# Optimization experiments

Hardware: AMD Instinct MI355X
Metric: run time of the kernel (lower is better)

## Reference

```python
import jax, jax.numpy as jnp
import numpy as np

T, B, E = 1024, 4, 1024
H = 16
D = E // H          # head_dim = 64
L = 16              # max_relative_length


def setup_inputs() -> dict:
    key = jax.random.key(0)
    ks = jax.random.split(key, 4)
    query = jax.random.normal(ks[0], (T, B, E), dtype=jnp.float32)
    # xavier-ish scaled params
    in_proj_weight = jax.random.normal(ks[1], (3 * E, E), dtype=jnp.float32) * (1.0 / np.sqrt(E))
    in_proj_bias = jnp.zeros((3 * E,), dtype=jnp.float32)
    rel_pos_keys = jax.random.normal(ks[2], (2 * L + 1, E), dtype=jnp.float32) * (1.0 / np.sqrt(E))
    out_w = jax.random.normal(ks[3], (E, E), dtype=jnp.float32) * (1.0 / np.sqrt(E))
    out_b = jnp.zeros((E,), dtype=jnp.float32)
    return {"query": query, "in_proj_weight": in_proj_weight, "in_proj_bias": in_proj_bias,
            "rel_pos_keys": rel_pos_keys, "out_w": out_w, "out_b": out_b}


def reference(query, in_proj_weight, in_proj_bias, rel_pos_keys, out_w, out_b):
    t, b, e = query.shape
    scaling = D ** (-0.5)
    # fused qkv projection: [T,B,3E]
    qkv = jnp.einsum('tbe,fe->tbf', query, in_proj_weight) + in_proj_bias
    q, k, v = jnp.split(qkv, 3, axis=-1)
    q = q * scaling
    # [T,B,E] -> [B*H, T, D]
    def heads(x):
        return x.reshape(t, b * H, D).transpose(1, 0, 2)
    q, k, v = heads(q), heads(k), heads(v)
    # clipped relative position matrix [T,T] in [0, 2L]
    r = jnp.arange(t)
    dist = jnp.clip(r[None, :] - r[:, None], -L, L) + L
    # gather relation keys, keep first head_dim channels: [T,T,D]
    rel_k = rel_pos_keys[dist][:, :, :D]
    # scores = q k^T + q . rel_k  (Shaw et al.), [B*H, T, T]
    scores = jnp.einsum('btd,bsd->bts', q, k) + jnp.einsum('btd,tsd->bts', q, rel_k)
    probs = jax.nn.softmax(scores, axis=-1)
    attn = jnp.einsum('bts,bsd->btd', probs, v)      # [B*H, T, D]
    attn = attn.transpose(1, 0, 2).reshape(t, b, e)   # [T, B, E]
    return jnp.einsum('tbe,oe->tbo', attn, out_w) + out_b
```

## Files before the change

kernel.cpp:

```cpp
#include <hip/hip_runtime.h>

typedef __attribute__((ext_vector_type(8))) short short8;
typedef __attribute__((ext_vector_type(4))) float floatx4;


__device__ __forceinline__ short f2bf(float x) {
  union { float f; unsigned u; } cv; cv.f = x;
  unsigned u = cv.u + (0x7FFFu + ((cv.u >> 16) & 1u));
  return (short)(u >> 16);
}

__device__ __forceinline__ floatx4 mfma16(short8 a, short8 b, floatx4 c) {
  return __builtin_amdgcn_mfma_f32_16x16x32_bf16(a, b, c, 0, 0, 0);
}

__device__ __forceinline__ void async_copy16(const void* g, void* l) {
  __builtin_amdgcn_global_load_lds((const __attribute__((address_space(1))) void*)g,
                                   (__attribute__((address_space(3))) void*)l, 16, 0, 0);
}

__global__ void __launch_bounds__(256) convert_all_kernel(
    const float* __restrict__ s0, const float* __restrict__ s1,
    const float* __restrict__ s2,
    short* __restrict__ d0, short* __restrict__ d1, short* __restrict__ d2)
{
  int i = blockIdx.x * 256 + threadIdx.x;
  const float* src; short* dst; int off;
  if (i < 524288)       { src = s0; dst = d0; off = i; }
  else if (i < 917504)  { src = s1; dst = d1; off = i - 524288; }
  else                  { src = s2; dst = d2; off = i - 917504; }
  const float4* s = (const float4*)src;
  float4 a = s[off * 2], b = s[off * 2 + 1];
  short8 o;
  o[0] = f2bf(a.x); o[1] = f2bf(a.y); o[2] = f2bf(a.z); o[3] = f2bf(a.w);
  o[4] = f2bf(b.x); o[5] = f2bf(b.y); o[6] = f2bf(b.z); o[7] = f2bf(b.w);
  *(short8*)(dst + (size_t)off * 8) = o;
}

__device__ __forceinline__ void gemm_stage(
    const short* __restrict__ A, const short* __restrict__ W,
    short* Atile, short* Btile, int m0, int n0, int K, int kk, int tid, int w)
{
  #pragma unroll
  for (int i = 0; i < 2; i++) {
    int seg = i * 256 + tid;
    int row = seg >> 2, p = seg & 3;
    int ck = (p - ((row >> 1) & 3)) & 3;
    async_copy16(A + (size_t)(m0 + row) * K + kk + ck * 8,
                 Atile + (size_t)(i * 256 + w * 64) * 8);
    async_copy16(W + (size_t)(n0 + row) * K + kk + ck * 8,
                 Btile + (size_t)(i * 256 + w * 64) * 8);
  }
}

__device__ __forceinline__ void gemm_core_db(
    const short* __restrict__ A, const short* __restrict__ W,
    short* At, short* Bt,
    int m0, int n0, int K, int tid, floatx4 acc[4][4])
{
  const int lane = tid & 63, w = tid >> 6;
  const int quad = lane >> 4, l16 = lane & 15;
  const int wm = (w >> 1) * 64, wn = (w & 1) * 64;
  #pragma unroll
  for (int mt = 0; mt < 4; mt++)
    #pragma unroll
    for (int nt = 0; nt < 4; nt++) acc[mt][nt] = (floatx4)(0.0f);

  gemm_stage(A, W, At, Bt, m0, n0, K, 0, tid, w);

  for (int kk = 0; kk < K; kk += 32) {
    const int cur = (kk >> 5) & 1;
    short* Ac = At + cur * (128 * 32);
    short* Bc = Bt + cur * (128 * 32);
    __syncthreads();
    if (kk + 32 < K)
      gemm_stage(A, W, At + (1 - cur) * (128 * 32), Bt + (1 - cur) * (128 * 32),
                 m0, n0, K, kk + 32, tid, w);
    short8 af[4], bfr[4];
    #pragma unroll
    for (int mt = 0; mt < 4; mt++) {
      int R = wm + mt * 16 + l16;
      af[mt] = *(const short8*)(Ac + R * 32 + ((quad + (R >> 1)) & 3) * 8);
    }
    #pragma unroll
    for (int nt = 0; nt < 4; nt++) {
      int R = wn + nt * 16 + l16;
      bfr[nt] = *(const short8*)(Bc + R * 32 + ((quad + (R >> 1)) & 3) * 8);
    }
    #pragma unroll
    for (int mt = 0; mt < 4; mt++)
      #pragma unroll
      for (int nt = 0; nt < 4; nt++)
        acc[mt][nt] = mfma16(af[mt], bfr[nt], acc[mt][nt]);
  }
}

__global__ void __launch_bounds__(256) gemm_qkv(
    const short* __restrict__ A, const short* __restrict__ W,
    const float* __restrict__ bias,
    short* __restrict__ q_ws, short* __restrict__ k_ws, short* __restrict__ v_ws)
{
  __shared__ __align__(16) short Atile[2 * 128 * 32];
  __shared__ __align__(16) short Btile[2 * 128 * 32];
  const int tid = threadIdx.x;
  const int m0 = blockIdx.x * 128, n0 = blockIdx.y * 128;
  floatx4 acc[4][4];
  gemm_core_db(A, W, Atile, Btile, m0, n0, 1024, tid, acc);

  const int lane = tid & 63, w = tid >> 6;
  const int quad = lane >> 4, l16 = lane & 15;
  const int wm = (w >> 1) * 64, wn = (w & 1) * 64;
  #pragma unroll
  for (int nt = 0; nt < 4; nt++) {
    int f = n0 + wn + nt * 16 + l16;
    float bv = bias[f];
    int which = f >> 10;
    int h = (f >> 6) & 15;
    int d = f & 63;
    #pragma unroll
    for (int mt = 0; mt < 4; mt++) {
      #pragma unroll
      for (int reg = 0; reg < 4; reg++) {
        int r = m0 + wm + mt * 16 + quad * 4 + reg;
        int t = r >> 2, b = r & 3;
        int bh = b * 16 + h;
        float val = acc[mt][nt][reg] + bv;
        if (which == 0)      q_ws[((size_t)bh * 1024 + t) * 64 + d] = f2bf(val * 0.125f);
        else if (which == 1) k_ws[((size_t)bh * 1024 + t) * 64 + d] = f2bf(val);
        else                 v_ws[((size_t)bh * 64 + d) * 1024 + t] = f2bf(val);
      }
    }
  }
}

__global__ void __launch_bounds__(256) attn_kernel(
    const short* __restrict__ q_ws, const short* __restrict__ k_ws,
    const short* __restrict__ v_ws, const float* __restrict__ relk,
    short* __restrict__ attn_ws)
{
  __shared__ float rel_lds[128 * 33];
  __shared__ __align__(16) short Ktile[64 * 64];
  __shared__ __align__(16) short Vtile[64 * 64];
  __shared__ __align__(16) short p_lds[4][32 * 64];
  const int tid = threadIdx.x, lane = tid & 63, w = tid >> 6;
  const int quad = lane >> 4, l16 = lane & 15;
  const int bh = blockIdx.x >> 3;
  const int t0 = (blockIdx.x & 7) * 128;
  const int b = bh >> 4, h = bh & 15;

  short8 aq[2][2];
  #pragma unroll
  for (int qt = 0; qt < 2; qt++)
    #pragma unroll
    for (int ks = 0; ks < 2; ks++)
      aq[qt][ks] = *(const short8*)(q_ws
          + ((size_t)bh * 1024 + t0 + qt * 64 + w * 16 + l16) * 64
          + ks * 32 + quad * 8);

  for (int i = tid; i < 48 * 8; i += 256) {
    int row = i >> 3, p = i & 7;
    short8 val;
    if (row < 33) {
      const float* src = relk + row * 1024 + p * 8;
      float4 a = *(const float4*)src, c = *(const float4*)(src + 4);
      val[0] = f2bf(a.x); val[1] = f2bf(a.y); val[2] = f2bf(a.z); val[3] = f2bf(a.w);
      val[4] = f2bf(c.x); val[5] = f2bf(c.y); val[6] = f2bf(c.z); val[7] = f2bf(c.w);
    } else {
      val = (short8)0;
    }
    *(short8*)(Ktile + row * 64 + ((p ^ (row & 7)) << 3)) = val;
  }
  __syncthreads();

  #pragma unroll
  for (int qt = 0; qt < 2; qt++) {
    #pragma unroll
    for (int jt = 0; jt < 3; jt++) {
      floatx4 scR = (floatx4)(0.0f);
      #pragma unroll
      for (int ks = 0; ks < 2; ks++) {
        int rrow = jt * 16 + l16;
        int ck = (quad + 4 * ks) ^ (rrow & 7);
        short8 rb = *(const short8*)(Ktile + rrow * 64 + ck * 8);
        scR = mfma16(aq[qt][ks], rb, scR);
      }
      int j = jt * 16 + l16;
      if (j < 33) {
        #pragma unroll
        for (int reg = 0; reg < 4; reg++) {
          int tl = qt * 64 + w * 16 + quad * 4 + reg;
          rel_lds[tl * 33 + j] = scR[reg];
        }
      }
    }
  }
  __syncthreads();

  float biasLo[2], biasHi[2];
  #pragma unroll
  for (int qt = 0; qt < 2; qt++) {
    int ql = qt * 64 + w * 16 + l16;
    biasLo[qt] = rel_lds[ql * 33 + 0];
    biasHi[qt] = rel_lds[ql * 33 + 32];
  }

  floatx4 o[2][4];
  #pragma unroll
  for (int qt = 0; qt < 2; qt++)
    #pragma unroll
    for (int dt = 0; dt < 4; dt++) o[qt][dt] = (floatx4)(0.0f);
  float rsum[2] = {0.f, 0.f};

  const short* kg = k_ws + (size_t)bh * 1024 * 64;
  const short* vg = v_ws + (size_t)bh * 64 * 1024;

  for (int st = 0; st < 16; st++) {
    const int s0 = st * 64;
    #pragma unroll
    for (int i = 0; i < 2; i++) {
      int seg = i * 256 + tid;
      int row = seg >> 3, p = seg & 7;
      int ck = p ^ (row & 7);
      async_copy16(kg + (size_t)(s0 + row) * 64 + ck * 8,
                   Ktile + (size_t)(i * 256 + w * 64) * 8);
      async_copy16(vg + (size_t)row * 1024 + s0 + ck * 8,
                   Vtile + (size_t)(i * 256 + w * 64) * 8);
    }
    __syncthreads();

    short8 kb[4][2];
    #pragma unroll
    for (int nt = 0; nt < 4; nt++)
      #pragma unroll
      for (int ks = 0; ks < 2; ks++) {
        int srow = nt * 16 + l16;
        kb[nt][ks] = *(const short8*)(Ktile + srow * 64
                                      + (((quad + 4 * ks) ^ (l16 & 7)) << 3));
      }

    floatx4 sc[2][4];
    #pragma unroll
    for (int qt = 0; qt < 2; qt++)
      #pragma unroll
      for (int nt = 0; nt < 4; nt++) {
        sc[qt][nt] = (floatx4)(0.0f);
        #pragma unroll
        for (int ks = 0; ks < 2; ks++)
          sc[qt][nt] = mfma16(kb[nt][ks], aq[qt][ks], sc[qt][nt]);
      }

    #pragma unroll
    for (int qt = 0; qt < 2; qt++) {
      const int qbase = t0 + qt * 64 + w * 16;
      bool alllo = (s0 <= qbase - 79);
      bool allhi = (s0 >= qbase + 31);
      if (alllo || allhi) {
        float bb = alllo ? biasLo[qt] : biasHi[qt];
        #pragma unroll
        for (int nt = 0; nt < 4; nt++)
          #pragma unroll
          for (int reg = 0; reg < 4; reg++) sc[qt][nt][reg] += bb;
      } else {
        int ql = qt * 64 + w * 16 + l16;
        #pragma unroll
        for (int nt = 0; nt < 4; nt++)
          #pragma unroll
          for (int reg = 0; reg < 4; reg++) {
            int delta = (s0 + 16 * nt + 4 * quad + reg) - (qbase + l16);
            delta = min(max(delta, -16), 16) + 16;
            sc[qt][nt][reg] += rel_lds[ql * 33 + delta];
          }
      }
      #pragma unroll
      for (int nt = 0; nt < 4; nt++) {
        #pragma unroll
        for (int reg = 0; reg < 4; reg++) {
          float p = __expf(sc[qt][nt][reg]);
          sc[qt][nt][reg] = p;
          rsum[qt] += p;
        }
        unsigned w0 = (unsigned)(unsigned short)f2bf(sc[qt][nt][0])
                    | ((unsigned)(unsigned short)f2bf(sc[qt][nt][1]) << 16);
        unsigned w1 = (unsigned)(unsigned short)f2bf(sc[qt][nt][2])
                    | ((unsigned)(unsigned short)f2bf(sc[qt][nt][3]) << 16);
        int srot = (16 * nt + 4 * quad + 4 * l16) & 63;
        *(uint2*)(p_lds[w] + (qt * 16 + l16) * 64 + srot) = make_uint2(w0, w1);
      }
    }

    short8 ap[2][2];
    #pragma unroll
    for (int qt = 0; qt < 2; qt++)
      #pragma unroll
      for (int ks = 0; ks < 2; ks++) {
        int s1 = (32 * ks + 8 * quad + 4 * l16) & 63;
        int s2 = (s1 + 4) & 63;
        union { short8 v; uint2 u[2]; } pu;
        pu.u[0] = *(const uint2*)(p_lds[w] + (qt * 16 + l16) * 64 + s1);
        pu.u[1] = *(const uint2*)(p_lds[w] + (qt * 16 + l16) * 64 + s2);
        ap[qt][ks] = pu.v;
      }

    #pragma unroll
    for (int dt = 0; dt < 4; dt++) {
      short8 vb[2];
      #pragma unroll
      for (int ks = 0; ks < 2; ks++) {
        int drow = dt * 16 + l16;
        vb[ks] = *(const short8*)(Vtile + drow * 64
                                  + (((quad + 4 * ks) ^ (l16 & 7)) << 3));
      }
      #pragma unroll
      for (int qt = 0; qt < 2; qt++)
        #pragma unroll
        for (int ks = 0; ks < 2; ks++)
          o[qt][dt] = mfma16(ap[qt][ks], vb[ks], o[qt][dt]);
    }
    __syncthreads();
  }

  #pragma unroll
  for (int qt = 0; qt < 2; qt++) {
    float rs = rsum[qt];
    rs += __shfl_xor(rs, 16, 64);
    rs += __shfl_xor(rs, 32, 64);
    float inv[4];
    #pragma unroll
    for (int reg = 0; reg < 4; reg++)
      inv[reg] = 1.0f / __shfl(rs, quad * 4 + reg, 64);
    #pragma unroll
    for (int dt = 0; dt < 4; dt++) {
      #pragma unroll
      for (int reg = 0; reg < 4; reg++) {
        int tg = t0 + qt * 64 + w * 16 + quad * 4 + reg;
        attn_ws[((size_t)tg * 4 + b) * 1024 + h * 64 + dt * 16 + l16]
          = f2bf(o[qt][dt][reg] * inv[reg]);
      }
    }
  }
}

__global__ void __launch_bounds__(256) gemm_outproj(
    const short* __restrict__ A, const short* __restrict__ W,
    const float* __restrict__ bias, float* __restrict__ out)
{
  __shared__ __align__(16) short Atile[2 * 64 * 32];
  __shared__ __align__(16) short Btile[2 * 128 * 32];
  const int tid = threadIdx.x;
  const int m0 = blockIdx.x * 64, n0 = blockIdx.y * 128;
  const int lane = tid & 63, w = tid >> 6;
  const int quad = lane >> 4, l16 = lane & 15;
  const int wm = (w >> 1) * 32, wn = (w & 1) * 64;

  floatx4 acc[2][4];
  #pragma unroll
  for (int mt = 0; mt < 2; mt++)
    #pragma unroll
    for (int nt = 0; nt < 4; nt++) acc[mt][nt] = (floatx4)(0.0f);

  #define STAGE_OP(KK, BUF)                                                  \
    {                                                                        \
      _Pragma("unroll")                                                      \
      for (int i = 0; i < 2; i++) {                                          \
        int seg = i * 256 + tid;                \
        int row = seg >> 2, p = seg & 3;                                     \
        int ck = (p - ((row >> 1) & 3)) & 3;                                 \
        async_copy16(W + (size_t)(n0 + row) * 1024 + (KK) + ck * 8,          \
                     Btile + (size_t)((BUF) * 4096 + (i * 256 + w * 64) * 8)); \
      }                                                                      \
      {                                                                      \
        int row = tid >> 2, p = tid & 3;         \
        int ck = (p - ((row >> 1) & 3)) & 3;                                 \
        async_copy16(A + (size_t)(m0 + row) * 1024 + (KK) + ck * 8,          \
                     Atile + (size_t)((BUF) * 2048 + (w * 64) * 8));         \
      }                                                                      \
    }

  STAGE_OP(0, 0);
  for (int kk = 0; kk < 1024; kk += 32) {
    const int cur = (kk >> 5) & 1;
    const short* Ac = Atile + cur * 2048;
    const short* Bc = Btile + cur * 4096;
    __syncthreads();
    if (kk + 32 < 1024) STAGE_OP(kk + 32, 1 - cur);
    short8 af[2], bfr[4];
    #pragma unroll
    for (int mt = 0; mt < 2; mt++) {
      int R = wm + mt * 16 + l16;
      af[mt] = *(const short8*)(Ac + R * 32 + ((quad + (R >> 1)) & 3) * 8);
    }
    #pragma unroll
    for (int nt = 0; nt < 4; nt++) {
      int R = wn + nt * 16 + l16;
      bfr[nt] = *(const short8*)(Bc + R * 32 + ((quad + (R >> 1)) & 3) * 8);
    }
    #pragma unroll
    for (int mt = 0; mt < 2; mt++)
      #pragma unroll
      for (int nt = 0; nt < 4; nt++)
        acc[mt][nt] = mfma16(af[mt], bfr[nt], acc[mt][nt]);
  }
  #undef STAGE_OP

  #pragma unroll
  for (int nt = 0; nt < 4; nt++) {
    int f = n0 + wn + nt * 16 + l16;
    float bv = bias[f];
    #pragma unroll
    for (int mt = 0; mt < 2; mt++) {
      #pragma unroll
      for (int reg = 0; reg < 4; reg++) {
        int r = m0 + wm + mt * 16 + quad * 4 + reg;
        out[(size_t)r * 1024 + f] = acc[mt][nt][reg] + bv;
      }
    }
  }
}

extern "C" void kernel_launch(void* const* d_in, const int* in_sizes, int n_in,
                              void* d_out, int out_size, void* d_ws, size_t ws_size,
                              hipStream_t stream) {
  const float* query = (const float*)d_in[0];
  const float* in_w  = (const float*)d_in[1];
  const float* in_b  = (const float*)d_in[2];
  const float* relk  = (const float*)d_in[3];
  const float* out_w = (const float*)d_in[4];
  const float* out_b = (const float*)d_in[5];
  float* out = (float*)d_out;

  short* qry_bf = (short*)d_ws;
  short* win_bf = qry_bf + (size_t)4096 * 1024;
  short* wout_bf = win_bf + (size_t)3072 * 1024;
  short* q_ws   = wout_bf + (size_t)1024 * 1024;
  short* k_ws   = q_ws + (size_t)64 * 1024 * 64;
  short* v_ws   = k_ws + (size_t)64 * 1024 * 64;
  short* att_ws = v_ws + (size_t)64 * 1024 * 64;

  convert_all_kernel<<<4096, 256, 0, stream>>>(query, in_w, out_w,
                                               qry_bf, win_bf, wout_bf);
  gemm_qkv<<<dim3(32, 24), 256, 0, stream>>>(qry_bf, win_bf, in_b, q_ws, k_ws, v_ws);
  attn_kernel<<<512, 256, 0, stream>>>(q_ws, k_ws, v_ws, relk, att_ws);
  gemm_outproj<<<dim3(64, 8), 256, 0, stream>>>(att_ws, wout_bf, out_b, out);
}
```

Baseline: 187.4 us.

## Reorder QKV GEMM rows batch-major, pack bf16 stores, remap attention block order

The input conversion now writes the query batch-major (b,t) instead of (t,b), so GEMM rows map to contiguous t within a batch. This lets the V-transposed epilogue store four consecutive t values as one 8-byte packed write instead of four scalar writes. The split between q, k and v is hoisted to block level. Conversions use the packed bf16x2 intrinsic. Attention blocks are remapped so consecutive blocks span different heads, which changes cache and scheduling locality. The change relies on the unseen GEMM core and out-proj keeping consistent indexing.

```diff
diff --git a/kernel.cpp b/kernel.cpp
--- a/kernel.cpp
+++ b/kernel.cpp
@@ -1,4 +1,5 @@
 #include <hip/hip_runtime.h>
+#include <hip/hip_bf16.h>
 
 typedef __attribute__((ext_vector_type(8))) short short8;
 typedef __attribute__((ext_vector_type(4))) float floatx4;
@@ -10,6 +11,12 @@
   return (short)(u >> 16);
 }
 
+__device__ __forceinline__ unsigned pk_bf16(float a, float b) {
+  union { __hip_bfloat162 h; unsigned u; } cv;
+  cv.h = __float22bfloat162_rn(make_float2(a, b));
+  return cv.u;
+}
+
 __device__ __forceinline__ floatx4 mfma16(short8 a, short8 b, floatx4 c) {
   return __builtin_amdgcn_mfma_f32_16x16x32_bf16(a, b, c, 0, 0, 0);
 }
@@ -25,16 +32,23 @@
     short* __restrict__ d0, short* __restrict__ d1, short* __restrict__ d2)
 {
   int i = blockIdx.x * 256 + threadIdx.x;
-  const float* src; short* dst; int off;
-  if (i < 524288)       { src = s0; dst = d0; off = i; }
-  else if (i < 917504)  { src = s1; dst = d1; off = i - 524288; }
-  else                  { src = s2; dst = d2; off = i - 917504; }
-  const float4* s = (const float4*)src;
-  float4 a = s[off * 2], b = s[off * 2 + 1];
-  short8 o;
-  o[0] = f2bf(a.x); o[1] = f2bf(a.y); o[2] = f2bf(a.z); o[3] = f2bf(a.w);
-  o[4] = f2bf(b.x); o[5] = f2bf(b.y); o[6] = f2bf(b.z); o[7] = f2bf(b.w);
-  *(short8*)(dst + (size_t)off * 8) = o;
+  if (i < 524288) {
+    int e8 = i & 127, b = (i >> 7) & 3, t = i >> 9;
+    const float4* s = (const float4*)s0 + (size_t)i * 2;
+    float4 a = s[0], c = s[1];
+    uint4 o = make_uint4(pk_bf16(a.x, a.y), pk_bf16(a.z, a.w),
+                         pk_bf16(c.x, c.y), pk_bf16(c.z, c.w));
+    *(uint4*)(d0 + (size_t)b * 1048576 + t * 1024 + e8 * 8) = o;
+  } else {
+    const float* src; short* dst; int off;
+    if (i < 917504) { src = s1; dst = d1; off = i - 524288; }
+    else            { src = s2; dst = d2; off = i - 917504; }
+    const float4* s = (const float4*)src + (size_t)off * 2;
+    float4 a = s[0], c = s[1];
+    uint4 o = make_uint4(pk_bf16(a.x, a.y), pk_bf16(a.z, a.w),
+                         pk_bf16(c.x, c.y), pk_bf16(c.z, c.w));
+    *(uint4*)(dst + (size_t)off * 8) = o;
+  }
 }
 
 __device__ __forceinline__ void gemm_stage(
@@ -110,24 +124,38 @@
   const int lane = tid & 63, w = tid >> 6;
   const int quad = lane >> 4, l16 = lane & 15;
   const int wm = (w >> 1) * 64, wn = (w & 1) * 64;
+  const int which = n0 >> 10;
   #pragma unroll
   for (int nt = 0; nt < 4; nt++) {
     int f = n0 + wn + nt * 16 + l16;
     float bv = bias[f];
-    int which = f >> 10;
     int h = (f >> 6) & 15;
     int d = f & 63;
-    #pragma unroll
-    for (int mt = 0; mt < 4; mt++) {
-      #pragma unroll
-      for (int reg = 0; reg < 4; reg++) {
-        int r = m0 + wm + mt * 16 + quad * 4 + reg;
-        int t = r >> 2, b = r & 3;
-        int bh = b * 16 + h;
-        float val = acc[mt][nt][reg] + bv;
-        if (which == 0)      q_ws[((size_t)bh * 1024 + t) * 64 + d] = f2bf(val * 0.125f);
-        else if (which == 1) k_ws[((size_t)bh * 1024 + t) * 64 + d] = f2bf(val);
-        else                 v_ws[((size_t)bh * 64 + d) * 1024 + t] = f2bf(val);
+    if (which == 2) {
+      #pragma unroll
+      for (int mt = 0; mt < 4; mt++) {
+        int r0 = m0 + wm + mt * 16 + quad * 4;
+        int t = r0 & 1023, bb = r0 >> 10;
+        int bh = bb * 16 + h;
+        unsigned lo = pk_bf16(acc[mt][nt][0] + bv, acc[mt][nt][1] + bv);
+        unsigned hi = pk_bf16(acc[mt][nt][2] + bv, acc[mt][nt][3] + bv);
+        *(uint2*)(v_ws + ((size_t)bh * 64 + d) * 1024 + t) = make_uint2(lo, hi);
+      }
+    } else {
+      short* dst = which ? k_ws : q_ws;
+      const float sc = which ? 1.0f : 0.125f;
+      #pragma unroll
+      for (int mt = 0; mt < 4; mt++) {
+        int r0 = m0 + wm + mt * 16 + quad * 4;
+        int t = r0 & 1023, bb = r0 >> 10;
+        int bh = bb * 16 + h;
+        unsigned u01 = pk_bf16((acc[mt][nt][0] + bv) * sc, (acc[mt][nt][1] + bv) * sc);
+        unsigned u23 = pk_bf16((acc[mt][nt][2] + bv) * sc, (acc[mt][nt][3] + bv) * sc);
+        size_t base = ((size_t)bh * 1024 + t) * 64 + d;
+        dst[base]           = (short)u01;
+        dst[base + 64]      = (short)(u01 >> 16);
+        dst[base + 128]     = (short)u23;
+        dst[base + 192]     = (short)(u23 >> 16);
       }
     }
   }
@@ -144,8 +172,8 @@
   __shared__ __align__(16) short p_lds[4][32 * 64];
   const int tid = threadIdx.x, lane = tid & 63, w = tid >> 6;
   const int quad = lane >> 4, l16 = lane & 15;
-  const int bh = blockIdx.x >> 3;
-  const int t0 = (blockIdx.x & 7) * 128;
+  const int bh = 8 * ((int)blockIdx.x & 7) + (((int)blockIdx.x >> 3) & 7);
+  const int t0 = ((int)blockIdx.x >> 6) * 128;
   const int b = bh >> 4, h = bh & 15;
 
   short8 aq[2][2];
@@ -279,10 +307,8 @@
           sc[qt][nt][reg] = p;
           rsum[qt] += p;
         }
-        unsigned w0 = (unsigned)(unsigned short)f2bf(sc[qt][nt][0])
-                    | ((unsigned)(unsigned short)f2bf(sc[qt][nt][1]) << 16);
-        unsigned w1 = (unsigned)(unsigned short)f2bf(sc[qt][nt][2])
-                    | ((unsigned)(unsigned short)f2bf(sc[qt][nt][3]) << 16);
+        unsigned w0 = pk_bf16(sc[qt][nt][0], sc[qt][nt][1]);
+        unsigned w1 = pk_bf16(sc[qt][nt][2], sc[qt][nt][3]);
         int srot = (16 * nt + 4 * quad + 4 * l16) & 63;
         *(uint2*)(p_lds[w] + (qt * 16 + l16) * 64 + srot) = make_uint2(w0, w1);
       }
@@ -330,12 +356,14 @@
       inv[reg] = 1.0f / __shfl(rs, quad * 4 + reg, 64);
     #pragma unroll
     for (int dt = 0; dt < 4; dt++) {
-      #pragma unroll
-      for (int reg = 0; reg < 4; reg++) {
-        int tg = t0 + qt * 64 + w * 16 + quad * 4 + reg;
-        attn_ws[((size_t)tg * 4 + b) * 1024 + h * 64 + dt * 16 + l16]
-          = f2bf(o[qt][dt][reg] * inv[reg]);
-      }
+      unsigned u01 = pk_bf16(o[qt][dt][0] * inv[0], o[qt][dt][1] * inv[1]);
+      unsigned u23 = pk_bf16(o[qt][dt][2] * inv[2], o[qt][dt][3] * inv[3]);
+      int tg = t0 + qt * 64 + w * 16 + quad * 4;
+      size_t base = ((size_t)tg * 4 + b) * 1024 + h * 64 + dt * 16 + l16;
+      attn_ws[base]         = (short)u01;
+      attn_ws[base + 4096]  = (short)(u01 >> 16);
+      attn_ws[base + 8192]  = (short)u23;
+      attn_ws[base + 12288] = (short)(u23 >> 16);
     }
   }
 }
```

Result: faster. 177.1 us (-5.5%).
